# Performance work log

Hardware: AMD Instinct MI355X
Metric: run time of the kernel (lower is better)

The kernel has to match this reference:

```python
import jax, jax.numpy as jnp
import numpy as np

HEADS = 16
DIM_HEAD = 64
EPS = 1e-5


def _layernorm(x, w, b):
    mu = jnp.mean(x, axis=-1, keepdims=True)
    var = jnp.var(x, axis=-1, keepdims=True)
    return (x - mu) * jax.lax.rsqrt(var + EPS) * w + b


def setup_inputs() -> dict:
    key = jax.random.key(0)
    ks = jax.random.split(key, 6)
    B, F, Q, D = 8, 4096, 64, 1024
    inner = HEADS * DIM_HEAD  # 1024
    s = 0.02
    return {
        "features": jax.random.normal(ks[0], (B, F, D), jnp.float32),
        "latents": jax.random.normal(ks[1], (B, Q, D), jnp.float32),
        "lnm_w": jnp.ones((D,), jnp.float32),
        "lnm_b": jnp.zeros((D,), jnp.float32),
        "lnl_w": jnp.ones((D,), jnp.float32),
        "lnl_b": jnp.zeros((D,), jnp.float32),
        "Wq": jax.random.normal(ks[2], (D, inner), jnp.float32) * s,
        "Wk": jax.random.normal(ks[3], (D, inner), jnp.float32) * s,
        "Wv": jax.random.normal(ks[4], (D, inner), jnp.float32) * s,
        "Wo": jax.random.normal(ks[5], (inner, D), jnp.float32) * s,
    }


def reference(features, latents, lnm_w, lnm_b, lnl_w, lnl_b, Wq, Wk, Wv, Wo):
    B, Q = latents.shape[0], latents.shape[1]
    scale = DIM_HEAD ** (-0.5)

    x = _layernorm(features, lnm_w, lnm_b)           # (B, F, D)
    lat = _layernorm(latents, lnl_w, lnl_b)          # (B, Q, D)

    q = (lat @ Wq).reshape(B, Q, HEADS, DIM_HEAD).transpose(0, 2, 1, 3)  # b h q d
    kv_in = jnp.concatenate([x, lat], axis=1)        # (B, F+Q, D)
    FL = kv_in.shape[1]
    k = (kv_in @ Wk).reshape(B, FL, HEADS, DIM_HEAD).transpose(0, 2, 1, 3)  # b h f d
    v = (kv_in @ Wv).reshape(B, FL, HEADS, DIM_HEAD).transpose(0, 2, 1, 3)  # b h f d

    sim = jnp.einsum('bhqd,bhfd->bhqf', q * scale, k)
    alphas = jax.nn.softmax(sim, axis=-1)            # amax-subtract is folded into stable softmax
    out = jnp.einsum('bhqf,bhfv->bhqv', alphas, v)
    out = out.transpose(0, 2, 1, 3).reshape(B, Q, HEADS * DIM_HEAD)
    return out @ Wo
```

## Files before the change

### kernel.cpp

```cpp
#include <hip/hip_runtime.h>


typedef float   f32x4  __attribute__((ext_vector_type(4)));
typedef short   bf16x8 __attribute__((ext_vector_type(8)));

#define MFMA_BF16 __builtin_amdgcn_mfma_f32_16x16x32_bf16

__device__ __forceinline__ unsigned short f2bf(float f) {
  unsigned u = __float_as_uint(f);
  unsigned r = (u + 0x7fffu + ((u >> 16) & 1u)) >> 16;
  return (unsigned short)r;
}

__device__ __forceinline__ void gload_lds16(const unsigned short* g, unsigned short* l) {
  __builtin_amdgcn_global_load_lds(
      (const __attribute__((address_space(1))) unsigned int*)g,
      (__attribute__((address_space(3))) unsigned int*)l, 16, 0, 0);
}

__global__ __launch_bounds__(256) void ln_kernel(
    const float* __restrict__ features, const float* __restrict__ latents,
    const float* __restrict__ lnm_w, const float* __restrict__ lnm_b,
    const float* __restrict__ lnl_w, const float* __restrict__ lnl_b,
    unsigned short* __restrict__ kv_ln, unsigned short* __restrict__ lat_ln)
{
  const int row = blockIdx.x;
  const int b  = row / 4160;
  const int fi = row - b * 4160;
  const bool is_lat = fi >= 4096;
  const float* x = is_lat ? (latents + (size_t)(b * 64 + fi - 4096) * 1024)
                          : (features + (size_t)(b * 4096 + fi) * 1024);
  const float* wp = is_lat ? lnl_w : lnm_w;
  const float* bp = is_lat ? lnl_b : lnm_b;
  const int tid = threadIdx.x;

  float4 v = *(const float4*)(x + tid * 4);
  float s  = v.x + v.y + v.z + v.w;
  float s2 = v.x * v.x + v.y * v.y + v.z * v.z + v.w * v.w;
#pragma unroll
  for (int sh = 1; sh < 64; sh <<= 1) {
    s  += __shfl_xor(s,  sh, 64);
    s2 += __shfl_xor(s2, sh, 64);
  }
  __shared__ float red[8];
  if ((tid & 63) == 0) { red[tid >> 6] = s; red[4 + (tid >> 6)] = s2; }
  __syncthreads();
  s  = red[0] + red[1] + red[2] + red[3];
  s2 = red[4] + red[5] + red[6] + red[7];
  const float mu   = s * (1.0f / 1024.0f);
  const float var  = s2 * (1.0f / 1024.0f) - mu * mu;
  const float rstd = rsqrtf(var + 1e-5f);

  float4 w4 = *(const float4*)(wp + tid * 4);
  float4 b4 = *(const float4*)(bp + tid * 4);
  ushort4 o;
  o.x = f2bf((v.x - mu) * rstd * w4.x + b4.x);
  o.y = f2bf((v.y - mu) * rstd * w4.y + b4.y);
  o.z = f2bf((v.z - mu) * rstd * w4.z + b4.z);
  o.w = f2bf((v.w - mu) * rstd * w4.w + b4.w);
  *(ushort4*)(kv_ln + (size_t)row * 1024 + tid * 4) = o;
  if (is_lat)
    *(ushort4*)(lat_ln + (size_t)(b * 64 + fi - 4096) * 1024 + tid * 4) = o;
}

__global__ __launch_bounds__(256) void wcast_kernel(
    const float* __restrict__ Wq, const float* __restrict__ Wk,
    const float* __restrict__ Wv, const float* __restrict__ Wo,
    unsigned short* __restrict__ Wkv_t, unsigned short* __restrict__ Wq_t,
    unsigned short* __restrict__ Wo_t)
{
  __shared__ float tile[32][33];
  const int kt = blockIdx.x * 32, nt = blockIdx.y * 32;
  const int tx = threadIdx.x & 31, ty = threadIdx.x >> 5;

  const float* src; int nc; float scale = 1.0f;
  if (nt < 1024)      { src = Wk; nc = nt; }
  else if (nt < 2048) { src = Wv; nc = nt - 1024; }
  else if (nt < 3072) { src = Wq; nc = nt - 2048; scale = 0.125f; }
  else                { src = Wo; nc = nt - 3072; }

#pragma unroll
  for (int kk = 0; kk < 4; ++kk)
    tile[ty + kk * 8][tx] = src[(size_t)(kt + ty + kk * 8) * 1024 + nc + tx] * scale;
  __syncthreads();

#pragma unroll
  for (int nn = 0; nn < 4; ++nn) {
    const int ng = nt + ty + nn * 8;
    unsigned short* d;
    if (ng < 2048)      d = Wkv_t + (size_t)ng * 1024;
    else if (ng < 3072) d = Wq_t + (size_t)(ng - 2048) * 1024;
    else                d = Wo_t + (size_t)(ng - 3072) * 1024;
    d[kt + tx] = f2bf(tile[tx][ty + nn * 8]);
  }
}

__global__ __launch_bounds__(512, 4) void gemm256_bf16(
    const unsigned short* __restrict__ A,
    const unsigned short* __restrict__ Bt,
    unsigned short* __restrict__ Kp, unsigned short* __restrict__ Vt,
    int M, int N, int K)
{
  __shared__ __align__(16) unsigned short lds[36864];
  const int tid  = threadIdx.x;
  const int wave = tid >> 6, lane = tid & 63;
  const int lo = lane & 15, hi = lane >> 4;
  const int wr = wave >> 1, wc = wave & 1;

  const int nbn = gridDim.x;
  int flat = blockIdx.y * nbn + blockIdx.x;
  const int nwg = nbn * gridDim.y;
  flat = (flat & 7) * (nwg >> 3) + (flat >> 3);
  const int bm = flat / nbn, bn = flat - bm * nbn;

  int garA[2], gakA[2];
#pragma unroll
  for (int gi = 0; gi < 2; ++gi) {
    int off = gi * 8192 + tid * 16;
    int p = off ^ (((off >> 9) & 1) << 5);
    int s = p >> 10, q = p & 1023;
    garA[gi] = (s >> 1) * 16 + (q >> 6) + 128 * (s & 1);
    gakA[gi] = (q & 63) >> 1;
  }
  int grB, gkB;
  {
    int off = tid * 16;
    int p = off ^ (((off >> 9) & 1) << 5);
    int s = p >> 10, q = p & 1023;
    grB = (s >> 1) * 16 + (q >> 6) + 64 * (s & 1);
    gkB = (q & 63) >> 1;
  }
  const unsigned short* pA0 = A  + (size_t)(bm * 256 + garA[0]) * K + gakA[0];
  const unsigned short* pA1 = A  + (size_t)(bm * 256 + garA[1]) * K + gakA[1];
  const unsigned short* pB  = Bt + (size_t)(bn * 128 + grB)     * K + gkB;

  f32x4 acc[4][4];
#pragma unroll
  for (int i = 0; i < 4; ++i)
#pragma unroll
    for (int j = 0; j < 4; ++j) acc[i][j] = (f32x4){0.f, 0.f, 0.f, 0.f};

  const int NT = K >> 5;

#pragma unroll
  for (int tt = 0; tt < 2; ++tt) {
    unsigned short* bb = lds + tt * 12288;
    gload_lds16(pA0 + tt * 32, bb + wave * 512);
    gload_lds16(pA1 + tt * 32, bb + 4096 + wave * 512);
    gload_lds16(pB  + tt * 32, bb + 8192 + wave * 512);
  }
  asm volatile("s_waitcnt vmcnt(3)" ::: "memory");
  asm volatile("s_barrier" ::: "memory");

  const int swz = (lo * 32 + hi * 8) ^ ((lo & 8) << 1);
  int aAddr[4], bAddr[4];
#pragma unroll
  for (int m = 0; m < 4; ++m)
    aAddr[m] = ((((wr & 1) * 4 + m) * 2) + (wr >> 1)) * 512 + swz;
#pragma unroll
  for (int n = 0; n < 4; ++n)
    bAddr[n] = 8192 + (n * 2 + wc) * 512 + swz;

  int cur = 0;
  for (int t = 0; t < NT; ++t) {
    const unsigned short* bp = lds + cur * 12288;
    bf16x8 af[4], bf[4];
#pragma unroll
    for (int m = 0; m < 4; ++m) af[m] = *(const bf16x8*)(bp + aAddr[m]);
#pragma unroll
    for (int n = 0; n < 4; ++n) bf[n] = *(const bf16x8*)(bp + bAddr[n]);

    if (t + 2 < NT) {
      int s2 = cur + 2; if (s2 >= 3) s2 -= 3;
      unsigned short* db = lds + s2 * 12288;
      const int koff = (t + 2) * 32;
      gload_lds16(pA0 + koff, db + wave * 512);
      gload_lds16(pA1 + koff, db + 4096 + wave * 512);
      gload_lds16(pB  + koff, db + 8192 + wave * 512);
    }

    __builtin_amdgcn_s_setprio(1);
#pragma unroll
    for (int m = 0; m < 4; ++m)
#pragma unroll
      for (int n = 0; n < 4; ++n)
        acc[m][n] = MFMA_BF16(af[m], bf[n], acc[m][n], 0, 0, 0);
    __builtin_amdgcn_s_setprio(0);

    if (t + 2 < NT)      { asm volatile("s_waitcnt vmcnt(3)" ::: "memory"); }
    else if (t + 1 < NT) { asm volatile("s_waitcnt vmcnt(0)" ::: "memory"); }
    asm volatile("s_barrier" ::: "memory");
    cur = (cur == 2) ? 0 : cur + 1;
  }

  if (bn < 8) {
#pragma unroll
    for (int m = 0; m < 4; ++m) {
      const int grow0 = bm * 256 + wr * 64 + m * 16 + hi * 4;
#pragma unroll
      for (int n = 0; n < 4; ++n) {
        const int gcol = bn * 128 + wc * 64 + n * 16 + lo;
        const size_t pbase = (size_t)(gcol >> 6) * 2129920 + (gcol & 63);
#pragma unroll
        for (int r = 0; r < 4; ++r)
          Kp[pbase + (size_t)(grow0 + r) * 64] = f2bf(acc[m][n][r]);
      }
    }
  } else {
    __syncthreads();
    unsigned short* ldsT = lds;
#pragma unroll
    for (int m = 0; m < 4; ++m) {
      const int row_l = wr * 64 + m * 16 + hi * 4;
#pragma unroll
      for (int n = 0; n < 4; ++n) {
        const int col_l = wc * 64 + n * 16 + lo;
#pragma unroll
        for (int r = 0; r < 4; ++r)
          ldsT[col_l * 264 + row_l + r] = f2bf(acc[m][n][r]);
      }
    }
    __syncthreads();
#pragma unroll
    for (int it = 0; it < 8; ++it) {
      const int col_l = it * 16 + (tid >> 5);
      const int rl = (tid & 31) * 8;
      bf16x8 v = *(const bf16x8*)&ldsT[col_l * 264 + rl];
      const int hcol = (bn - 8) * 128 + col_l;
      const size_t dst = (size_t)(hcol >> 6) * 2129920
                       + (size_t)(hcol & 63) * 33280 + bm * 256 + rl;
      *(bf16x8*)&Vt[dst] = v;
    }
  }
}

template <typename CT>
__global__ __launch_bounds__(256) void gemm_tn(
    const unsigned short* __restrict__ A,
    const unsigned short* __restrict__ Bt,
    CT* __restrict__ C, int M, int N, int K)
{
  __shared__ __align__(16) unsigned short sA[2][128 * 32];
  __shared__ __align__(16) unsigned short sB[2][128 * 32];
  const int tid  = threadIdx.x;
  const int wave = tid >> 6, lane = tid & 63;
  const int bm = blockIdx.y, bn = blockIdx.x;
  const int wr = wave >> 1, wc = wave & 1;
  const int lo = lane & 15, hi = lane >> 4;
  const int srow = lane >> 2, squad = lane & 3;

  const unsigned short* gA = A  + (size_t)(bm * 128 + srow) * K + squad * 8;
  const unsigned short* gB = Bt + (size_t)(bn * 128 + srow) * K + squad * 8;

  f32x4 acc[4][4];
#pragma unroll
  for (int i = 0; i < 4; ++i)
#pragma unroll
    for (int j = 0; j < 4; ++j) acc[i][j] = (f32x4){0.f, 0.f, 0.f, 0.f};

  const int kt = K >> 5;
#pragma unroll
  for (int c = 0; c < 2; ++c) {
    const int chunk = wave * 2 + c;
    gload_lds16(gA + (size_t)chunk * 16 * K, &sA[0][chunk * 512]);
    gload_lds16(gB + (size_t)chunk * 16 * K, &sB[0][chunk * 512]);
  }
  __syncthreads();

  int buf = 0;
  for (int t = 0; t < kt; ++t) {
    if (t + 1 < kt) {
      const int k0 = (t + 1) << 5;
#pragma unroll
      for (int c = 0; c < 2; ++c) {
        const int chunk = wave * 2 + c;
        gload_lds16(gA + (size_t)chunk * 16 * K + k0, &sA[buf ^ 1][chunk * 512]);
        gload_lds16(gB + (size_t)chunk * 16 * K + k0, &sB[buf ^ 1][chunk * 512]);
      }
    }
    bf16x8 af[4], bfr[4];
#pragma unroll
    for (int i = 0; i < 4; ++i) {
      af[i]  = *(const bf16x8*)&sA[buf][(wr * 64 + i * 16 + lo) * 32 + hi * 8];
      bfr[i] = *(const bf16x8*)&sB[buf][(wc * 64 + i * 16 + lo) * 32 + hi * 8];
    }
#pragma unroll
    for (int i = 0; i < 4; ++i)
#pragma unroll
      for (int j = 0; j < 4; ++j)
        acc[i][j] = MFMA_BF16(af[i], bfr[j], acc[i][j], 0, 0, 0);
    __syncthreads();
    buf ^= 1;
  }

#pragma unroll
  for (int i = 0; i < 4; ++i) {
    const int row0 = bm * 128 + wr * 64 + i * 16 + hi * 4;
#pragma unroll
    for (int j = 0; j < 4; ++j) {
      const int col = bn * 128 + wc * 64 + j * 16 + lo;
#pragma unroll
      for (int r = 0; r < 4; ++r) {
        const size_t idx = (size_t)(row0 + r) * N + col;
        if constexpr (sizeof(CT) == 2) C[idx] = (CT)f2bf(acc[i][j][r]);
        else                            C[idx] = acc[i][j][r];
      }
    }
  }
}

__global__ __launch_bounds__(256) void attn_kernel(
    const unsigned short* __restrict__ qws,
    const unsigned short* __restrict__ Kp, const unsigned short* __restrict__ Vt,
    float* __restrict__ pacc, float* __restrict__ pml)
{
  const int bhs = blockIdx.x;
  const int s = bhs & 7, h = (bhs >> 3) & 15, b = bhs >> 7;
  const int t0 = (s * 65) >> 3;
  const int t1 = ((s + 1) * 65) >> 3;
  const int tid = threadIdx.x;
  const int wave = tid >> 6, lane = tid & 63;
  const int lo = lane & 15, hi = lane >> 4;

  __shared__ __align__(16) unsigned short sK [64][72];
  __shared__ __align__(16) unsigned short sVT[64][72];
  __shared__ __align__(16) unsigned short sP [4][16][72];

  bf16x8 qf[2];
  {
    const unsigned short* p = qws + (size_t)(b * 64 + wave * 16 + lo) * 1024 + h * 64 + hi * 8;
    qf[0] = *(const bf16x8*)p;
    qf[1] = *(const bf16x8*)(p + 32);
  }
  float m[4] = {-1e30f, -1e30f, -1e30f, -1e30f};
  float l[4] = {0.f, 0.f, 0.f, 0.f};
  f32x4 acc[4];
#pragma unroll
  for (int i = 0; i < 4; ++i) acc[i] = (f32x4){0.f, 0.f, 0.f, 0.f};

  const int frow = tid >> 2, c4 = tid & 3;
  const int vd = tid >> 3, vfo = (tid & 7) * 8;
  const size_t hbase = (size_t)h * 2129920;

  bf16x8 kreg[2], vreg[2];
  {
    const size_t rowb = (size_t)(b * 4160 + t0 * 64);
#pragma unroll
    for (int rr = 0; rr < 2; ++rr)
      kreg[rr] = *(const bf16x8*)(Kp + hbase + (rowb + frow) * 64 + rr * 32 + c4 * 8);
#pragma unroll
    for (int p = 0; p < 2; ++p)
      vreg[p] = *(const bf16x8*)(Vt + hbase + (size_t)(vd + p * 32) * 33280 + rowb + vfo);
  }

  for (int t = t0; t < t1; ++t) {
    __syncthreads();
#pragma unroll
    for (int rr = 0; rr < 2; ++rr)
      *(bf16x8*)&sK[frow][rr * 32 + c4 * 8] = kreg[rr];
#pragma unroll
    for (int p = 0; p < 2; ++p)
      *(bf16x8*)&sVT[vd + p * 32][vfo] = vreg[p];
    __syncthreads();
    if (t + 1 < t1) {
      const size_t rowb = (size_t)(b * 4160 + (t + 1) * 64);
#pragma unroll
      for (int rr = 0; rr < 2; ++rr)
        kreg[rr] = *(const bf16x8*)(Kp + hbase + (rowb + frow) * 64 + rr * 32 + c4 * 8);
#pragma unroll
      for (int p = 0; p < 2; ++p)
        vreg[p] = *(const bf16x8*)(Vt + hbase + (size_t)(vd + p * 32) * 33280 + rowb + vfo);
    }

    f32x4 sim[4];
#pragma unroll
    for (int nf = 0; nf < 4; ++nf) {
      f32x4 a0 = (f32x4){0.f, 0.f, 0.f, 0.f};
#pragma unroll
      for (int ks = 0; ks < 2; ++ks) {
        bf16x8 kf = *(const bf16x8*)&sK[nf * 16 + lo][ks * 32 + hi * 8];
        a0 = MFMA_BF16(qf[ks], kf, a0, 0, 0, 0);
      }
      sim[nf] = a0;
    }

    float pr[4][4];
    float corr[4];
#pragma unroll
    for (int r = 0; r < 4; ++r) {
      float tm = fmaxf(fmaxf(sim[0][r], sim[1][r]), fmaxf(sim[2][r], sim[3][r]));
#pragma unroll
      for (int sh = 1; sh < 16; sh <<= 1) tm = fmaxf(tm, __shfl_xor(tm, sh, 64));
      const float mn = fmaxf(m[r], tm);
      corr[r] = __expf(m[r] - mn);
      float rs = 0.f;
#pragma unroll
      for (int nf = 0; nf < 4; ++nf) {
        float p = __expf(sim[nf][r] - mn);
        pr[r][nf] = p;
        rs += p;
      }
#pragma unroll
      for (int sh = 1; sh < 16; sh <<= 1) rs += __shfl_xor(rs, sh, 64);
      l[r] = l[r] * corr[r] + rs;
      m[r] = mn;
    }

    {
      const int r2 = lane & 3;
      float csel = r2 == 0 ? corr[0] : r2 == 1 ? corr[1] : r2 == 2 ? corr[2] : corr[3];
      const int src = ((lane & 15) >> 2) * 16 + (lane & 3);
      const float cacc = __shfl(csel, src, 64);
#pragma unroll
      for (int i = 0; i < 4; ++i) acc[i] *= cacc;
    }

#pragma unroll
    for (int r = 0; r < 4; ++r)
#pragma unroll
      for (int nf = 0; nf < 4; ++nf)
        sP[wave][hi * 4 + r][nf * 16 + lo] = f2bf(pr[r][nf]);

#pragma unroll
    for (int ks = 0; ks < 2; ++ks) {
      bf16x8 pf = *(const bf16x8*)&sP[wave][lo][ks * 32 + hi * 8];
#pragma unroll
      for (int i = 0; i < 4; ++i) {
        bf16x8 vf = *(const bf16x8*)&sVT[i * 16 + lo][ks * 32 + hi * 8];
        acc[i] = MFMA_BF16(vf, pf, acc[i], 0, 0, 0);
      }
    }
  }

  if (lo == 0) {
#pragma unroll
    for (int r = 0; r < 4; ++r) {
      pml[bhs * 128 + wave * 16 + hi * 4 + r]      = m[r];
      pml[bhs * 128 + 64 + wave * 16 + hi * 4 + r] = l[r];
    }
  }
#pragma unroll
  for (int i = 0; i < 4; ++i)
#pragma unroll
    for (int r = 0; r < 4; ++r)
      pacc[bhs * 4096 + (i * 16 + hi * 4 + r) * 64 + wave * 16 + lo] = acc[i][r];
}

__global__ __launch_bounds__(256) void attn_combine(
    const float* __restrict__ pacc, const float* __restrict__ pml,
    unsigned short* __restrict__ attn_out)
{
  const int bh = blockIdx.x;
  const int b = bh >> 4, h = bh & 15;
  const int t = threadIdx.x;
  const int q = t & 63, dg = t >> 6;
  const int base = bh << 3;

  float mm[8], ll[8];
#pragma unroll
  for (int s = 0; s < 8; ++s) {
    mm[s] = pml[(base + s) * 128 + q];
    ll[s] = pml[(base + s) * 128 + 64 + q];
  }
  float M = mm[0];
#pragma unroll
  for (int s = 1; s < 8; ++s) M = fmaxf(M, mm[s]);
  float e[8];
  float L = 0.f;
#pragma unroll
  for (int s = 0; s < 8; ++s) { e[s] = __expf(mm[s] - M); L += e[s] * ll[s]; }
  const float inv = 1.0f / L;

#pragma unroll
  for (int dd = 0; dd < 16; ++dd) {
    const int d = dg * 16 + dd;
    float v = 0.f;
#pragma unroll
    for (int s = 0; s < 8; ++s)
      v += e[s] * pacc[(base + s) * 4096 + d * 64 + q];
    attn_out[(size_t)(b * 64 + q) * 1024 + h * 64 + d] = f2bf(v * inv);
  }
}

extern "C" void kernel_launch(void* const* d_in, const int* in_sizes, int n_in,
                              void* d_out, int out_size, void* d_ws, size_t ws_size,
                              hipStream_t stream) {
  const float* features = (const float*)d_in[0];
  const float* latents  = (const float*)d_in[1];
  const float* lnm_w = (const float*)d_in[2];
  const float* lnm_b = (const float*)d_in[3];
  const float* lnl_w = (const float*)d_in[4];
  const float* lnl_b = (const float*)d_in[5];
  const float* Wq = (const float*)d_in[6];
  const float* Wk = (const float*)d_in[7];
  const float* Wv = (const float*)d_in[8];
  const float* Wo = (const float*)d_in[9];
  float* out = (float*)d_out;

  char* ws = (char*)d_ws;
  unsigned short* kv_ln    = (unsigned short*)(ws);
  unsigned short* Wkv_t    = (unsigned short*)(ws + 68157440);
  unsigned short* Wq_t     = (unsigned short*)(ws + 72351744);
  unsigned short* Wo_t     = (unsigned short*)(ws + 74448896);
  unsigned short* lat_ln   = (unsigned short*)(ws + 76546048);
  unsigned short* q_ws     = (unsigned short*)(ws + 77594624);
  unsigned short* attn_out = (unsigned short*)(ws + 78643200);
  unsigned short* Kp       = (unsigned short*)(ws + 79691776);
  unsigned short* Vt       = (unsigned short*)(ws + 147849216);
  float* pacc = (float*)(ws);
  float* pml  = (float*)(ws + 16777216);

  ln_kernel<<<33280, 256, 0, stream>>>(features, latents, lnm_w, lnm_b, lnl_w, lnl_b,
                                       kv_ln, lat_ln);
  wcast_kernel<<<dim3(32, 128), 256, 0, stream>>>(Wq, Wk, Wv, Wo, Wkv_t, Wq_t, Wo_t);
  gemm256_bf16<<<dim3(16, 130), 512, 0, stream>>>(kv_ln, Wkv_t, Kp, Vt, 33280, 2048, 1024);
  gemm_tn<unsigned short><<<dim3(8, 4), 256, 0, stream>>>(lat_ln, Wq_t, q_ws, 512, 1024, 1024);
  attn_kernel<<<1024, 256, 0, stream>>>(q_ws, Kp, Vt, pacc, pml);
  attn_combine<<<128, 256, 0, stream>>>(pacc, pml, attn_out);
  gemm_tn<float><<<dim3(8, 4), 256, 0, stream>>>(attn_out, Wo_t, out, 512, 1024, 1024);
}
```

Baseline: 285.1 us.

## Load GEMM B fragments directly from global into registers instead of LDS

Measured after the change: 683.5 us. +139.8%, slower.

```diff
diff --git a/kernel.cpp b/kernel.cpp
--- a/kernel.cpp
+++ b/kernel.cpp
@@ -101,7 +101,7 @@
     unsigned short* __restrict__ Kp, unsigned short* __restrict__ Vt,
     int M, int N, int K)
 {
-  __shared__ __align__(16) unsigned short lds[36864];
+  __shared__ __align__(16) unsigned short lds[33792];
   const int tid  = threadIdx.x;
   const int wave = tid >> 6, lane = tid & 63;
   const int lo = lane & 15, hi = lane >> 4;
@@ -122,17 +122,13 @@
     garA[gi] = (s >> 1) * 16 + (q >> 6) + 128 * (s & 1);
     gakA[gi] = (q & 63) >> 1;
   }
-  int grB, gkB;
-  {
-    int off = tid * 16;
-    int p = off ^ (((off >> 9) & 1) << 5);
-    int s = p >> 10, q = p & 1023;
-    grB = (s >> 1) * 16 + (q >> 6) + 64 * (s & 1);
-    gkB = (q & 63) >> 1;
-  }
-  const unsigned short* pA0 = A  + (size_t)(bm * 256 + garA[0]) * K + gakA[0];
-  const unsigned short* pA1 = A  + (size_t)(bm * 256 + garA[1]) * K + gakA[1];
-  const unsigned short* pB  = Bt + (size_t)(bn * 128 + grB)     * K + gkB;
+  const unsigned short* pA0 = A + (size_t)(bm * 256 + garA[0]) * K + gakA[0];
+  const unsigned short* pA1 = A + (size_t)(bm * 256 + garA[1]) * K + gakA[1];
+
+  const unsigned short* pBf[4];
+#pragma unroll
+  for (int n2 = 0; n2 < 4; ++n2)
+    pBf[n2] = Bt + (size_t)(bn * 128 + wc * 64 + n2 * 16 + lo) * K + hi * 8;
 
   f32x4 acc[4][4];
 #pragma unroll
@@ -142,56 +138,61 @@
 
   const int NT = K >> 5;
 
-#pragma unroll
-  for (int tt = 0; tt < 2; ++tt) {
-    unsigned short* bb = lds + tt * 12288;
-    gload_lds16(pA0 + tt * 32, bb + wave * 512);
-    gload_lds16(pA1 + tt * 32, bb + 4096 + wave * 512);
-    gload_lds16(pB  + tt * 32, bb + 8192 + wave * 512);
-  }
-  asm volatile("s_waitcnt vmcnt(3)" ::: "memory");
+  gload_lds16(pA0,      lds + wave * 512);
+  gload_lds16(pA1,      lds + 4096 + wave * 512);
+  gload_lds16(pA0 + 32, lds + 8192 + wave * 512);
+  gload_lds16(pA1 + 32, lds + 8192 + 4096 + wave * 512);
+  __builtin_amdgcn_sched_barrier(0);
+  bf16x8 bA[4], bB[4];
+#pragma unroll
+  for (int n2 = 0; n2 < 4; ++n2) bA[n2] = *(const bf16x8*)(pBf[n2]);
+  __builtin_amdgcn_sched_barrier(0);
+  asm volatile("s_waitcnt vmcnt(6)" ::: "memory");
   asm volatile("s_barrier" ::: "memory");
 
   const int swz = (lo * 32 + hi * 8) ^ ((lo & 8) << 1);
-  int aAddr[4], bAddr[4];
+  int aAddr[4];
 #pragma unroll
   for (int m = 0; m < 4; ++m)
     aAddr[m] = ((((wr & 1) * 4 + m) * 2) + (wr >> 1)) * 512 + swz;
-#pragma unroll
-  for (int n = 0; n < 4; ++n)
-    bAddr[n] = 8192 + (n * 2 + wc) * 512 + swz;
 
   int cur = 0;
-  for (int t = 0; t < NT; ++t) {
-    const unsigned short* bp = lds + cur * 12288;
-    bf16x8 af[4], bf[4];
-#pragma unroll
-    for (int m = 0; m < 4; ++m) af[m] = *(const bf16x8*)(bp + aAddr[m]);
-#pragma unroll
-    for (int n = 0; n < 4; ++n) bf[n] = *(const bf16x8*)(bp + bAddr[n]);
-
-    if (t + 2 < NT) {
-      int s2 = cur + 2; if (s2 >= 3) s2 -= 3;
-      unsigned short* db = lds + s2 * 12288;
-      const int koff = (t + 2) * 32;
-      gload_lds16(pA0 + koff, db + wave * 512);
-      gload_lds16(pA1 + koff, db + 4096 + wave * 512);
-      gload_lds16(pB  + koff, db + 8192 + wave * 512);
-    }
-
-    __builtin_amdgcn_s_setprio(1);
-#pragma unroll
-    for (int m = 0; m < 4; ++m)
-#pragma unroll
-      for (int n = 0; n < 4; ++n)
-        acc[m][n] = MFMA_BF16(af[m], bf[n], acc[m][n], 0, 0, 0);
-    __builtin_amdgcn_s_setprio(0);
-
-    if (t + 2 < NT)      { asm volatile("s_waitcnt vmcnt(3)" ::: "memory"); }
-    else if (t + 1 < NT) { asm volatile("s_waitcnt vmcnt(0)" ::: "memory"); }
-    asm volatile("s_barrier" ::: "memory");
-    cur = (cur == 2) ? 0 : cur + 1;
-  }
+
+#define GTILE(T, BUSE, BNEW)                                                   \
+  do {                                                                         \
+    const unsigned short* bp = lds + cur * 8192;                               \
+    bf16x8 af[4];                                                              \
+    _Pragma("unroll") for (int m2 = 0; m2 < 4; ++m2)                           \
+      af[m2] = *(const bf16x8*)(bp + aAddr[m2]);                               \
+    if ((T) + 1 < NT) {                                                        \
+      _Pragma("unroll") for (int n2 = 0; n2 < 4; ++n2)                         \
+        BNEW[n2] = *(const bf16x8*)(pBf[n2] + ((T) + 1) * 32);                 \
+    }                                                                          \
+    __builtin_amdgcn_sched_barrier(0);                                         \
+    if ((T) + 2 < NT) {                                                        \
+      int s2 = cur + 2; if (s2 >= 3) s2 -= 3;                                  \
+      unsigned short* db = lds + s2 * 8192;                                    \
+      const int koff = ((T) + 2) * 32;                                         \
+      gload_lds16(pA0 + koff, db + wave * 512);                                \
+      gload_lds16(pA1 + koff, db + 4096 + wave * 512);                         \
+    }                                                                          \
+    __builtin_amdgcn_sched_barrier(0);                                         \
+    __builtin_amdgcn_s_setprio(1);                                             \
+    _Pragma("unroll") for (int m2 = 0; m2 < 4; ++m2)                           \
+      _Pragma("unroll") for (int n2 = 0; n2 < 4; ++n2)                         \
+        acc[m2][n2] = MFMA_BF16(af[m2], BUSE[n2], acc[m2][n2], 0, 0, 0);       \
+    __builtin_amdgcn_s_setprio(0);                                             \
+    if ((T) + 2 < NT)      { asm volatile("s_waitcnt vmcnt(6)" ::: "memory"); }\
+    else if ((T) + 1 < NT) { asm volatile("s_waitcnt vmcnt(0)" ::: "memory"); }\
+    asm volatile("s_barrier" ::: "memory");                                    \
+    cur = (cur == 2) ? 0 : cur + 1;                                            \
+  } while (0)
+
+  for (int t = 0; t < NT; t += 2) {
+    GTILE(t,     bA, bB);
+    GTILE(t + 1, bB, bA);
+  }
+#undef GTILE
 
   if (bn < 8) {
 #pragma unroll
```
